# Performance work log

Measured on AMD Instinct MI355X. Metric: run time of the kernel, lower is better.

The kernel has to match this reference:

```python
import jax, jax.numpy as jnp
import numpy as np

H = 8              # n_heads
N_PER_GRAPH = 64   # nodes per graph (equal-sized graphs)


def setup_inputs() -> dict:
    key = jax.random.key(0)
    ks = jax.random.split(key, 5)
    total, D = 65536, 512
    x = jax.random.normal(ks[0], (total, D), dtype=jnp.float32)
    batch = jnp.arange(total, dtype=jnp.int64) // N_PER_GRAPH  # sorted graph ids
    s = 1.0 / np.sqrt(D).astype(np.float32)
    # nn.MultiheadAttention packed in-proj (xavier-ish uniform) + zero bias
    in_proj_w = jax.random.uniform(ks[1], (3 * D, D), jnp.float32, -s, s)
    in_proj_b = jnp.zeros((3 * D,), jnp.float32)
    out_proj_w = jax.random.uniform(ks[2], (D, D), jnp.float32, -s, s)
    out_proj_b = jnp.zeros((D,), jnp.float32)
    gate_w = jax.random.uniform(ks[3], (1, D), jnp.float32, -s, s)
    gate_b = jnp.zeros((1,), jnp.float32)
    return {"x": x, "batch": batch, "in_proj_w": in_proj_w, "in_proj_b": in_proj_b,
            "out_proj_w": out_proj_w, "out_proj_b": out_proj_b,
            "gate_w": gate_w, "gate_b": gate_b}


def reference(x, batch, in_proj_w, in_proj_b, out_proj_w, out_proj_b, gate_w, gate_b):
    total, D = x.shape
    G = total // N_PER_GRAPH
    hd = D // H
    xg = x.reshape(G, N_PER_GRAPH, D)                       # [G, N, D]
    # packed qkv projection (torch: x @ in_proj_w.T + in_proj_b)
    qkv = jnp.einsum('gnd,ed->gne', xg, in_proj_w) + in_proj_b
    q, k, v = jnp.split(qkv, 3, axis=-1)
    def to_heads(t):
        return t.reshape(G, N_PER_GRAPH, H, hd).transpose(0, 2, 1, 3)  # [G, H, N, hd]
    q, k, v = to_heads(q), to_heads(k), to_heads(v)
    scores = jnp.einsum('ghnd,ghmd->ghnm', q, k) * (1.0 / np.sqrt(hd))
    attn = jax.nn.softmax(scores, axis=-1)
    ctx = jnp.einsum('ghnm,ghmd->ghnd', attn, v)
    ctx = ctx.transpose(0, 2, 1, 3).reshape(G, N_PER_GRAPH, D)
    attn_out = jnp.einsum('gnd,ed->gne', ctx, out_proj_w) + out_proj_b  # [G, N, D]
    gates = jax.nn.sigmoid(jnp.einsum('gnd,od->gno', attn_out, gate_w) + gate_b)
    return (attn_out * gates).sum(axis=1)                   # [G, D]
```

## Files before the change

### kernel.cpp

```cpp
#include <hip/hip_runtime.h>
#include <stdint.h>


typedef __attribute__((ext_vector_type(8))) short short8;
typedef __attribute__((ext_vector_type(4))) float f32x4;

#define D_ 512

#define WQKV_OFF   0u
#define WO_OFF     1572864u
#define UPART_OFF  2097152u
#define U_OFF      2129920u
#define C0_OFF     2131968u
#define SG_OFF     2132032u
#define WCTX_OFF   2136128u

__device__ __forceinline__ unsigned short f2bf(float f) {
    union { float f; unsigned int u; } t; t.f = f;
    unsigned int u = t.u;
    return (unsigned short)((u + 0x7FFFu + ((u >> 16) & 1u)) >> 16);
}
__device__ __forceinline__ unsigned pack2(float a, float b) {
    return (unsigned)f2bf(a) | ((unsigned)f2bf(b) << 16);
}

__global__ __launch_bounds__(256)
void convert_weights(const float* __restrict__ wqkv, const float* __restrict__ wo,
                     unsigned short* __restrict__ wbf) {
    const int i4 = blockIdx.x * 256 + threadIdx.x;
    float4 v;
    if (i4 < 196608) v = *(const float4*)(wqkv + (size_t)i4 * 4);
    else             v = *(const float4*)(wo   + (size_t)(i4 - 196608) * 4);
    uint2 p; p.x = pack2(v.x, v.y); p.y = pack2(v.z, v.w);
    *(uint2*)(wbf + (size_t)i4 * 4) = p;
}

__global__ __launch_bounds__(256)
void compute_u_partial(const float* __restrict__ wo, const float* __restrict__ gw,
                       float* __restrict__ upart) {
    const int b = blockIdx.x;
    const int t = threadIdx.x;
    float a0 = 0.f, a1 = 0.f;
    #pragma unroll 4
    for (int e = b * 32; e < b * 32 + 32; ++e) {
        const float ge = gw[e];
        a0 += wo[(size_t)e * 512 + t]       * ge;
        a1 += wo[(size_t)e * 512 + t + 256] * ge;
    }
    upart[b * 512 + t] = a0; upart[b * 512 + t + 256] = a1;
}

__global__ __launch_bounds__(256)
void finalize_u(const float* __restrict__ upart, const float* __restrict__ bo,
                const float* __restrict__ gw, const float* __restrict__ gb,
                float* __restrict__ u, float* __restrict__ c0) {
    const int t = threadIdx.x;
    float s0 = 0.f, s1 = 0.f;
    #pragma unroll
    for (int b = 0; b < 16; ++b) { s0 += upart[b*512 + t]; s1 += upart[b*512 + t + 256]; }
    u[t] = s0; u[t + 256] = s1;
    __shared__ float rb[256];
    rb[t] = bo[t] * gw[t] + bo[t + 256] * gw[t + 256];
    __syncthreads();
    for (int s = 128; s > 0; s >>= 1) { if (t < s) rb[t] += rb[t + s]; __syncthreads(); }
    if (t == 0) c0[0] = rb[0] + gb[0];
}

union U8 { unsigned u[4]; short8 s; };

__global__ __launch_bounds__(512, 2)
void attn_ctx_kernel(const float* __restrict__ x,
                     const unsigned short* __restrict__ wqkv,
                     const float* __restrict__ bqkv,
                     const float* __restrict__ u,
                     const float* __restrict__ c0,
                     unsigned short* __restrict__ wctx_ws,
                     float* __restrict__ sumgate)
{
    __shared__ unsigned short xs[64][520];
    __shared__ unsigned short scr[8][64][72];
    __shared__ float logitp[8][64];
    __shared__ float gatev[64];

    const int g    = blockIdx.x;
    const int tid  = threadIdx.x;
    const int w    = tid >> 6;
    const int lane = tid & 63;
    const int l15  = lane & 15;
    const int quad = lane >> 4;

    #pragma unroll
    for (int i = 0; i < 16; ++i) {
        int idx = tid + i * 512;
        int row = idx >> 7;
        int c4  = idx & 127;
        float4 v = *(const float4*)(x + ((size_t)(g*64 + row))*512 + c4*4);
        uint2 p; p.x = pack2(v.x, v.y); p.y = pack2(v.z, v.w);
        *(uint2*)(&xs[row][c4*4]) = p;
    }
    __syncthreads();

    const int h = w;
    unsigned short (*S)[72] = scr[w];

    U8 qA[4][2], kB[4][2];
    #pragma unroll
    for (int dt = 0; dt < 4; ++dt) {
        f32x4 aq[4], ak[4], av[4];
        #pragma unroll
        for (int nt = 0; nt < 4; ++nt) {
            aq[nt] = (f32x4){0.f,0.f,0.f,0.f};
            ak[nt] = (f32x4){0.f,0.f,0.f,0.f};
            av[nt] = (f32x4){0.f,0.f,0.f,0.f};
        }
        const unsigned short* wq = wqkv + (size_t)(          h*64 + dt*16 + l15) * 512;
        const unsigned short* wk = wqkv + (size_t)( 512 +    h*64 + dt*16 + l15) * 512;
        const unsigned short* wv = wqkv + (size_t)(1024 +    h*64 + dt*16 + l15) * 512;
        #pragma unroll 4
        for (int ks = 0; ks < 16; ++ks) {
            const int col = ks*32 + quad*8;
            short8 a0 = *(const short8*)(wq + col);
            short8 a1 = *(const short8*)(wk + col);
            short8 a2 = *(const short8*)(wv + col);
            #pragma unroll
            for (int nt = 0; nt < 4; ++nt) {
                short8 b = *(const short8*)(&xs[nt*16 + l15][col]);
                aq[nt] = __builtin_amdgcn_mfma_f32_16x16x32_bf16(a0, b, aq[nt], 0,0,0);
                ak[nt] = __builtin_amdgcn_mfma_f32_16x16x32_bf16(a1, b, ak[nt], 0,0,0);
                av[nt] = __builtin_amdgcn_mfma_f32_16x16x32_bf16(a2, b, av[nt], 0,0,0);
            }
        }
        float bq[4], bk2[4], bv2[4];
        #pragma unroll
        for (int r = 0; r < 4; ++r) {
            bq[r]  = bqkv[          h*64 + dt*16 + quad*4 + r];
            bk2[r] = bqkv[ 512 +    h*64 + dt*16 + quad*4 + r];
            bv2[r] = bqkv[1024 +    h*64 + dt*16 + quad*4 + r];
        }
        const bool take = ((quad >> 1) == (dt & 1));
        const int  ks2  = dt >> 1;
        #pragma unroll
        for (int nt = 0; nt < 4; ++nt) {
            unsigned q01 = pack2(aq[nt][0]+bq[0],  aq[nt][1]+bq[1]);
            unsigned q23 = pack2(aq[nt][2]+bq[2],  aq[nt][3]+bq[3]);
            unsigned k01 = pack2(ak[nt][0]+bk2[0], ak[nt][1]+bk2[1]);
            unsigned k23 = pack2(ak[nt][2]+bk2[2], ak[nt][3]+bk2[3]);
            #pragma unroll
            for (int j = 0; j < 4; ++j) {
                int srcl = ((quad & 1)*2 + (j >> 1))*16 + l15;
                unsigned tq = (unsigned)__shfl((int)((j & 1) ? q23 : q01), srcl);
                unsigned tk = (unsigned)__shfl((int)((j & 1) ? k23 : k01), srcl);
                if (take) { qA[nt][ks2].u[j] = tq; kB[nt][ks2].u[j] = tk; }
            }
            #pragma unroll
            for (int r = 0; r < 4; ++r)
                S[dt*16 + quad*4 + r][nt*16 + l15] = f2bf(av[nt][r] + bv2[r]);
        }
    }

    f32x4 sacc[4][4];
    #pragma unroll
    for (int a = 0; a < 4; ++a)
        #pragma unroll
        for (int b = 0; b < 4; ++b) sacc[a][b] = (f32x4){0.f,0.f,0.f,0.f};
    #pragma unroll
    for (int ks2 = 0; ks2 < 2; ++ks2)
        #pragma unroll
        for (int a = 0; a < 4; ++a)
            #pragma unroll
            for (int b = 0; b < 4; ++b)
                sacc[a][b] = __builtin_amdgcn_mfma_f32_16x16x32_bf16(
                                 qA[a][ks2].s, kB[b][ks2].s, sacc[a][b], 0,0,0);

    #pragma unroll
    for (int a = 0; a < 4; ++a) {
        #pragma unroll
        for (int r = 0; r < 4; ++r) {
            float m0 = -1e30f;
            #pragma unroll
            for (int b = 0; b < 4; ++b) { sacc[a][b][r] *= 0.125f; m0 = fmaxf(m0, sacc[a][b][r]); }
            m0 = fmaxf(m0, __shfl_xor(m0, 1));
            m0 = fmaxf(m0, __shfl_xor(m0, 2));
            m0 = fmaxf(m0, __shfl_xor(m0, 4));
            m0 = fmaxf(m0, __shfl_xor(m0, 8));
            float s = 0.f;
            #pragma unroll
            for (int b = 0; b < 4; ++b) { float e = __expf(sacc[a][b][r] - m0); sacc[a][b][r] = e; s += e; }
            s += __shfl_xor(s, 1); s += __shfl_xor(s, 2); s += __shfl_xor(s, 4); s += __shfl_xor(s, 8);
            float inv = 1.0f / s;
            #pragma unroll
            for (int b = 0; b < 4; ++b) sacc[a][b][r] *= inv;
        }
    }

    U8 vA[4][2];
    #pragma unroll
    for (int dtile = 0; dtile < 4; ++dtile)
        #pragma unroll
        for (int ks2 = 0; ks2 < 2; ++ks2)
            vA[dtile][ks2].s = *(const short8*)(&S[dtile*16 + l15][ks2*32 + quad*8]);

    #pragma unroll
    for (int a = 0; a < 4; ++a)
        #pragma unroll
        for (int b = 0; b < 4; ++b)
            #pragma unroll
            for (int r = 0; r < 4; ++r)
                S[a*16 + quad*4 + r][b*16 + l15] = f2bf(sacc[a][b][r]);

    U8 pB[4][2];
    #pragma unroll
    for (int a = 0; a < 4; ++a)
        #pragma unroll
        for (int ks2 = 0; ks2 < 2; ++ks2)
            pB[a][ks2].s = *(const short8*)(&S[a*16 + l15][ks2*32 + quad*8]);

    f32x4 cacc[4][4];
    #pragma unroll
    for (int dtile = 0; dtile < 4; ++dtile)
        #pragma unroll
        for (int a = 0; a < 4; ++a) cacc[dtile][a] = (f32x4){0.f,0.f,0.f,0.f};
    #pragma unroll
    for (int ks2 = 0; ks2 < 2; ++ks2)
        #pragma unroll
        for (int dtile = 0; dtile < 4; ++dtile)
            #pragma unroll
            for (int a = 0; a < 4; ++a)
                cacc[dtile][a] = __builtin_amdgcn_mfma_f32_16x16x32_bf16(
                                     vA[dtile][ks2].s, pB[a][ks2].s, cacc[dtile][a], 0,0,0);

    {
        float uv[4][4];
        #pragma unroll
        for (int dtile = 0; dtile < 4; ++dtile)
            #pragma unroll
            for (int r = 0; r < 4; ++r)
                uv[dtile][r] = u[h*64 + dtile*16 + quad*4 + r];
        #pragma unroll
        for (int a = 0; a < 4; ++a) {
            float s = 0.f;
            #pragma unroll
            for (int dtile = 0; dtile < 4; ++dtile)
                #pragma unroll
                for (int r = 0; r < 4; ++r)
                    s += cacc[dtile][a][r] * uv[dtile][r];
            s += __shfl_xor(s, 16); s += __shfl_xor(s, 32);
            if (quad == 0) logitp[w][a*16 + l15] = s;
        }
    }
    __syncthreads();

    if (tid < 64) {
        float lg = c0[0];
        #pragma unroll
        for (int ww = 0; ww < 8; ++ww) lg += logitp[ww][tid];
        float gt = 1.0f / (1.0f + __expf(-lg));
        gatev[tid] = gt;
        float s = gt;
        s += __shfl_xor(s, 1);  s += __shfl_xor(s, 2);  s += __shfl_xor(s, 4);
        s += __shfl_xor(s, 8);  s += __shfl_xor(s, 16); s += __shfl_xor(s, 32);
        if (tid == 0) sumgate[g] = s;
    }
    __syncthreads();

    {
        float gv[4];
        #pragma unroll
        for (int a = 0; a < 4; ++a) gv[a] = gatev[a*16 + l15];
        #pragma unroll
        for (int dtile = 0; dtile < 4; ++dtile) {
            float sr[4];
            #pragma unroll
            for (int r = 0; r < 4; ++r) {
                float s = cacc[dtile][0][r]*gv[0] + cacc[dtile][1][r]*gv[1]
                        + cacc[dtile][2][r]*gv[2] + cacc[dtile][3][r]*gv[3];
                s += __shfl_xor(s, 1); s += __shfl_xor(s, 2);
                s += __shfl_xor(s, 4); s += __shfl_xor(s, 8);
                sr[r] = s;
            }
            if (l15 == 0) {
                uint2 pk; pk.x = pack2(sr[0], sr[1]); pk.y = pack2(sr[2], sr[3]);
                *(uint2*)(wctx_ws + (size_t)g*512 + h*64 + dtile*16 + quad*4) = pk;
            }
        }
    }
}

__global__ __launch_bounds__(256, 4)
void outproj_kernel(const unsigned short* __restrict__ wo_bf,
                    const unsigned short* __restrict__ wctx_bf,
                    const float* __restrict__ bo,
                    const float* __restrict__ sumgate,
                    float* __restrict__ out)
{
    const int tid  = threadIdx.x;
    const int w    = tid >> 6;
    const int lane = tid & 63;
    const int l15  = lane & 15;
    const int quad = lane >> 4;
    const int g0   = blockIdx.x * 32;

    f32x4 oac[8][2];
    #pragma unroll
    for (int et = 0; et < 8; ++et)
        #pragma unroll
        for (int mt = 0; mt < 2; ++mt)
            oac[et][mt] = (f32x4){0.f,0.f,0.f,0.f};

    #pragma unroll 4
    for (int ks = 0; ks < 16; ++ks) {
        const int col = ks*32 + quad*8;
        short8 a0 = *(const short8*)(wctx_bf + (size_t)(g0 + l15)*D_      + col);
        short8 a1 = *(const short8*)(wctx_bf + (size_t)(g0 + 16 + l15)*D_ + col);
        #pragma unroll
        for (int et = 0; et < 8; ++et) {
            short8 b = *(const short8*)(wo_bf + (size_t)(w*128 + et*16 + l15)*D_ + col);
            oac[et][0] = __builtin_amdgcn_mfma_f32_16x16x32_bf16(a0, b, oac[et][0], 0,0,0);
            oac[et][1] = __builtin_amdgcn_mfma_f32_16x16x32_bf16(a1, b, oac[et][1], 0,0,0);
        }
    }
    #pragma unroll
    for (int et = 0; et < 8; ++et) {
        const int e = w*128 + et*16 + l15;
        const float bov = bo[e];
        #pragma unroll
        for (int mt = 0; mt < 2; ++mt)
            #pragma unroll
            for (int r = 0; r < 4; ++r) {
                const int gg = g0 + mt*16 + quad*4 + r;
                out[(size_t)gg*D_ + e] = oac[et][mt][r] + sumgate[gg] * bov;
            }
    }
}

extern "C" void kernel_launch(void* const* d_in, const int* in_sizes, int n_in,
                              void* d_out, int out_size, void* d_ws, size_t ws_size,
                              hipStream_t stream) {
    const float* x    = (const float*)d_in[0];
    const float* wqkv = (const float*)d_in[2];
    const float* bqkv = (const float*)d_in[3];
    const float* wo   = (const float*)d_in[4];
    const float* bo   = (const float*)d_in[5];
    const float* gw   = (const float*)d_in[6];
    const float* gb   = (const float*)d_in[7];
    float* out = (float*)d_out;

    char* ws = (char*)d_ws;
    unsigned short* wqkv_bf = (unsigned short*)(ws + WQKV_OFF);
    unsigned short* wo_bf   = (unsigned short*)(ws + WO_OFF);
    float*          upart   = (float*)(ws + UPART_OFF);
    float*          u_ws    = (float*)(ws + U_OFF);
    float*          c0_ws   = (float*)(ws + C0_OFF);
    float*          sg_ws   = (float*)(ws + SG_OFF);
    unsigned short* wctx_ws = (unsigned short*)(ws + WCTX_OFF);

    const int total = in_sizes[0] / D_;
    const int G     = total / 64;

    hipLaunchKernelGGL(convert_weights,   dim3(1024), dim3(256), 0, stream, wqkv, wo, wqkv_bf);
    hipLaunchKernelGGL(compute_u_partial, dim3(16),   dim3(256), 0, stream, wo, gw, upart);
    hipLaunchKernelGGL(finalize_u,        dim3(1),    dim3(256), 0, stream, upart, bo, gw, gb, u_ws, c0_ws);
    hipLaunchKernelGGL(attn_ctx_kernel,   dim3(G),    dim3(512), 0, stream,
                       x, wqkv_bf, bqkv, u_ws, c0_ws, wctx_ws, sg_ws);
    hipLaunchKernelGGL(outproj_kernel,    dim3(G/32), dim3(256), 0, stream,
                       wo_bf, wctx_ws, bo, sg_ws, out);
}
```

Measured before the change: 444.9 us.

## Fold gate-vector prep into weight conversion and attention kernels; retile outproj grid

```diff
diff --git a/kernel.cpp b/kernel.cpp
--- a/kernel.cpp
+++ b/kernel.cpp
@@ -10,8 +10,6 @@
 #define WQKV_OFF   0u
 #define WO_OFF     1572864u
 #define UPART_OFF  2097152u
-#define U_OFF      2129920u
-#define C0_OFF     2131968u
 #define SG_OFF     2132032u
 #define WCTX_OFF   2136128u
 
@@ -26,7 +24,21 @@
 
 __global__ __launch_bounds__(256)
 void convert_weights(const float* __restrict__ wqkv, const float* __restrict__ wo,
-                     unsigned short* __restrict__ wbf) {
+                     unsigned short* __restrict__ wbf,
+                     const float* __restrict__ gw, float* __restrict__ upart) {
+    if (blockIdx.x >= 1024) {
+        const int b = blockIdx.x - 1024;
+        const int t = threadIdx.x;
+        float a0 = 0.f, a1 = 0.f;
+        #pragma unroll 4
+        for (int e = b * 32; e < b * 32 + 32; ++e) {
+            const float ge = gw[e];
+            a0 += wo[(size_t)e * 512 + t]       * ge;
+            a1 += wo[(size_t)e * 512 + t + 256] * ge;
+        }
+        upart[b * 512 + t] = a0; upart[b * 512 + t + 256] = a1;
+        return;
+    }
     const int i4 = blockIdx.x * 256 + threadIdx.x;
     float4 v;
     if (i4 < 196608) v = *(const float4*)(wqkv + (size_t)i4 * 4);
@@ -35,45 +47,16 @@
     *(uint2*)(wbf + (size_t)i4 * 4) = p;
 }
 
-__global__ __launch_bounds__(256)
-void compute_u_partial(const float* __restrict__ wo, const float* __restrict__ gw,
-                       float* __restrict__ upart) {
-    const int b = blockIdx.x;
-    const int t = threadIdx.x;
-    float a0 = 0.f, a1 = 0.f;
-    #pragma unroll 4
-    for (int e = b * 32; e < b * 32 + 32; ++e) {
-        const float ge = gw[e];
-        a0 += wo[(size_t)e * 512 + t]       * ge;
-        a1 += wo[(size_t)e * 512 + t + 256] * ge;
-    }
-    upart[b * 512 + t] = a0; upart[b * 512 + t + 256] = a1;
-}
-
-__global__ __launch_bounds__(256)
-void finalize_u(const float* __restrict__ upart, const float* __restrict__ bo,
-                const float* __restrict__ gw, const float* __restrict__ gb,
-                float* __restrict__ u, float* __restrict__ c0) {
-    const int t = threadIdx.x;
-    float s0 = 0.f, s1 = 0.f;
-    #pragma unroll
-    for (int b = 0; b < 16; ++b) { s0 += upart[b*512 + t]; s1 += upart[b*512 + t + 256]; }
-    u[t] = s0; u[t + 256] = s1;
-    __shared__ float rb[256];
-    rb[t] = bo[t] * gw[t] + bo[t + 256] * gw[t + 256];
-    __syncthreads();
-    for (int s = 128; s > 0; s >>= 1) { if (t < s) rb[t] += rb[t + s]; __syncthreads(); }
-    if (t == 0) c0[0] = rb[0] + gb[0];
-}
-
 union U8 { unsigned u[4]; short8 s; };
 
 __global__ __launch_bounds__(512, 2)
 void attn_ctx_kernel(const float* __restrict__ x,
                      const unsigned short* __restrict__ wqkv,
                      const float* __restrict__ bqkv,
-                     const float* __restrict__ u,
-                     const float* __restrict__ c0,
+                     const float* __restrict__ upart,
+                     const float* __restrict__ bo,
+                     const float* __restrict__ gw,
+                     const float* __restrict__ gb,
                      unsigned short* __restrict__ wctx_ws,
                      float* __restrict__ sumgate)
 {
@@ -81,6 +64,8 @@
     __shared__ unsigned short scr[8][64][72];
     __shared__ float logitp[8][64];
     __shared__ float gatev[64];
+    __shared__ float u_s[512];
+    __shared__ float c0_s;
 
     const int g    = blockIdx.x;
     const int tid  = threadIdx.x;
@@ -97,6 +82,20 @@
         float4 v = *(const float4*)(x + ((size_t)(g*64 + row))*512 + c4*4);
         uint2 p; p.x = pack2(v.x, v.y); p.y = pack2(v.z, v.w);
         *(uint2*)(&xs[row][c4*4]) = p;
+    }
+    {
+        float s = 0.f;
+        #pragma unroll
+        for (int b = 0; b < 16; ++b) s += upart[b*512 + tid];
+        u_s[tid] = s;
+    }
+    if (tid < 64) {
+        float s = 0.f;
+        #pragma unroll
+        for (int i = 0; i < 8; ++i) s += bo[tid*8 + i] * gw[tid*8 + i];
+        s += __shfl_xor(s, 1);  s += __shfl_xor(s, 2);  s += __shfl_xor(s, 4);
+        s += __shfl_xor(s, 8);  s += __shfl_xor(s, 16); s += __shfl_xor(s, 32);
+        if (tid == 0) c0_s = s + gb[0];
     }
     __syncthreads();
 
@@ -235,7 +234,7 @@
         for (int dtile = 0; dtile < 4; ++dtile)
             #pragma unroll
             for (int r = 0; r < 4; ++r)
-                uv[dtile][r] = u[h*64 + dtile*16 + quad*4 + r];
+                uv[dtile][r] = u_s[h*64 + dtile*16 + quad*4 + r];
         #pragma unroll
         for (int a = 0; a < 4; ++a) {
             float s = 0.f;
@@ -251,7 +250,7 @@
     __syncthreads();
 
     if (tid < 64) {
-        float lg = c0[0];
+        float lg = c0_s;
         #pragma unroll
         for (int ww = 0; ww < 8; ++ww) lg += logitp[ww][tid];
         float gt = 1.0f / (1.0f + __expf(-lg));
@@ -298,38 +297,23 @@
     const int lane = tid & 63;
     const int l15  = lane & 15;
     const int quad = lane >> 4;
-    const int g0   = blockIdx.x * 32;
-
-    f32x4 oac[8][2];
-    #pragma unroll
-    for (int et = 0; et < 8; ++et)
-        #pragma unroll
-        for (int mt = 0; mt < 2; ++mt)
-            oac[et][mt] = (f32x4){0.f,0.f,0.f,0.f};
-
+    const int g0   = blockIdx.x * 16;
+    const int e0   = blockIdx.y * 64;
+
+    f32x4 oac = (f32x4){0.f,0.f,0.f,0.f};
     #pragma unroll 4
     for (int ks = 0; ks < 16; ++ks) {
         const int col = ks*32 + quad*8;
-        short8 a0 = *(const short8*)(wctx_bf + (size_t)(g0 + l15)*D_      + col);
-        short8 a1 = *(const short8*)(wctx_bf + (size_t)(g0 + 16 + l15)*D_ + col);
-        #pragma unroll
-        for (int et = 0; et < 8; ++et) {
-            short8 b = *(const short8*)(wo_bf + (size_t)(w*128 + et*16 + l15)*D_ + col);
-            oac[et][0] = __builtin_amdgcn_mfma_f32_16x16x32_bf16(a0, b, oac[et][0], 0,0,0);
-            oac[et][1] = __builtin_amdgcn_mfma_f32_16x16x32_bf16(a1, b, oac[et][1], 0,0,0);
-        }
-    }
-    #pragma unroll
-    for (int et = 0; et < 8; ++et) {
-        const int e = w*128 + et*16 + l15;
-        const float bov = bo[e];
-        #pragma unroll
-        for (int mt = 0; mt < 2; ++mt)
-            #pragma unroll
-            for (int r = 0; r < 4; ++r) {
-                const int gg = g0 + mt*16 + quad*4 + r;
-                out[(size_t)gg*D_ + e] = oac[et][mt][r] + sumgate[gg] * bov;
-            }
+        short8 a = *(const short8*)(wctx_bf + (size_t)(g0 + l15)*D_ + col);
+        short8 b = *(const short8*)(wo_bf + (size_t)(e0 + w*16 + l15)*D_ + col);
+        oac = __builtin_amdgcn_mfma_f32_16x16x32_bf16(a, b, oac, 0,0,0);
+    }
+    const int e = e0 + w*16 + l15;
+    const float bov = bo[e];
+    #pragma unroll
+    for (int r = 0; r < 4; ++r) {
+        const int gg = g0 + quad*4 + r;
+        out[(size_t)gg*D_ + e] = oac[r] + sumgate[gg] * bov;
     }
 }
 
@@ -349,19 +333,16 @@
     unsigned short* wqkv_bf = (unsigned short*)(ws + WQKV_OFF);
     unsigned short* wo_bf   = (unsigned short*)(ws + WO_OFF);
     float*          upart   = (float*)(ws + UPART_OFF);
-    float*          u_ws    = (float*)(ws + U_OFF);
-    float*          c0_ws   = (float*)(ws + C0_OFF);
     float*          sg_ws   = (float*)(ws + SG_OFF);
     unsigned short* wctx_ws = (unsigned short*)(ws + WCTX_OFF);
 
     const int total = in_sizes[0] / D_;
     const int G     = total / 64;
 
-    hipLaunchKernelGGL(convert_weights,   dim3(1024), dim3(256), 0, stream, wqkv, wo, wqkv_bf);
-    hipLaunchKernelGGL(compute_u_partial, dim3(16),   dim3(256), 0, stream, wo, gw, upart);
-    hipLaunchKernelGGL(finalize_u,        dim3(1),    dim3(256), 0, stream, upart, bo, gw, gb, u_ws, c0_ws);
-    hipLaunchKernelGGL(attn_ctx_kernel,   dim3(G),    dim3(512), 0, stream,
-                       x, wqkv_bf, bqkv, u_ws, c0_ws, wctx_ws, sg_ws);
-    hipLaunchKernelGGL(outproj_kernel,    dim3(G/32), dim3(256), 0, stream,
+    hipLaunchKernelGGL(convert_weights, dim3(1040), dim3(256), 0, stream,
+                       wqkv, wo, wqkv_bf, gw, upart);
+    hipLaunchKernelGGL(attn_ctx_kernel, dim3(G), dim3(512), 0, stream,
+                       x, wqkv_bf, bqkv, upart, bo, gw, gb, wctx_ws, sg_ws);
+    hipLaunchKernelGGL(outproj_kernel, dim3(G/16, 8), dim3(256), 0, stream,
                        wo_bf, wctx_ws, bo, sg_ws, out);
 }
```

Result: faster. 423.5 us (-4.8%).
